# Performance work log

Measured on AMD Instinct MI355X. Metric: run time of the kernel, lower is better.

The kernel has to match this reference:

```python
import jax, jax.numpy as jnp
import numpy as np
from jax.scipy.special import logsumexp

B, S, D, L = 64, 512, 1024, 9


def setup_inputs() -> dict:
    key = jax.random.key(0)
    k1, k2, k3, k4, k5, k6 = jax.random.split(key, 6)
    inputs = jax.random.normal(k1, (B, S, D), dtype=jnp.float32)
    targets = jax.random.randint(k2, (B, S), 0, L)
    sequence_lengths = jax.random.randint(k3, (B,), S // 2, S + 1)
    mask = (jnp.arange(S)[None, :] < sequence_lengths[:, None])
    W = jax.random.normal(k4, (D, L), dtype=jnp.float32) * (1.0 / np.sqrt(D))
    b = jnp.zeros((L,), dtype=jnp.float32)
    transitions = jax.random.normal(k5, (L, L), dtype=jnp.float32) * 0.1
    return {"inputs": inputs, "targets": targets, "sequence_lengths": sequence_lengths,
            "mask": mask, "W": W, "b": b, "transitions": transitions}


def crf_nll(logits, tags, mask, transitions):
    # logits: [B,S,L], tags: [B,S] int, mask: [B,S] bool, transitions: [L,L]
    maskf = mask.astype(logits.dtype)
    # gold-path score (numerator)
    emit = jnp.take_along_axis(logits, tags[..., None], axis=2)[..., 0]  # [B,S]
    trans = transitions[tags[:, :-1], tags[:, 1:]]                        # [B,S-1]
    numerator = (emit * maskf).sum(-1) + (trans * maskf[:, 1:]).sum(-1)   # [B]
    # partition function via forward algorithm (scan over time)
    alpha0 = logits[:, 0]  # [B,L]; position 0 always valid
    emit_t = jnp.swapaxes(logits[:, 1:], 0, 1)   # [S-1,B,L]
    mask_t = jnp.swapaxes(mask[:, 1:], 0, 1)     # [S-1,B]

    def step(alpha, xs):
        e, m = xs
        scores = alpha[:, :, None] + transitions[None, :, :] + e[:, None, :]  # [B,L,L]
        new = logsumexp(scores, axis=1)                                        # [B,L]
        alpha = jnp.where(m[:, None], new, alpha)
        return alpha, None

    alpha, _ = jax.lax.scan(step, alpha0, (emit_t, mask_t))
    denominator = logsumexp(alpha, axis=-1)  # [B]
    return -(numerator - denominator).sum()


def reference(inputs, targets, sequence_lengths, mask, W, b, transitions):
    logits = jnp.einsum('bsd,dl->bsl', inputs, W) + b  # nn.Linear
    values = crf_nll(logits, targets, mask, transitions)
    return (values, logits)
```

## Files before the change

kernel.cpp:

```cpp
#include <hip/hip_runtime.h>
#include <hip/hip_bf16.h>
#include <math.h>

#define BB 64
#define SS 512
#define DD 1024
#define LL 9
#define NCHUNK 32
#define CLEN 16

#define DPP_ADD(v, ctrl)                                                     \
  v += __int_as_float(__builtin_amdgcn_update_dpp(                           \
      0, __float_as_int(v), ctrl, 0xF, 0xF, false))

__global__ __launch_bounds__(256) void gemm_kernel(
    const float* __restrict__ in, const float* __restrict__ W,
    const float* __restrict__ bias, float* __restrict__ out) {
  __shared__ float Wt[LL][DD];
  int tid = threadIdx.x;
  for (int i = tid; i < DD * LL; i += 256) {
    int k = i / LL, l = i - k * LL;
    Wt[l][k] = W[i];
  }
  __syncthreads();

  int lane = tid & 63;
  int wave = tid >> 6;
  int p = lane & 15;
  int sub = lane >> 4;

  int r0 = blockIdx.x * 64 + wave * 16 + sub;
  const float* x0 = in + (size_t)r0 * DD + p * 4;

  float acc[4][LL];
#pragma unroll
  for (int q = 0; q < 4; ++q)
#pragma unroll
    for (int l = 0; l < LL; ++l) acc[q][l] = 0.f;

  float4 a[4], an[4];
#pragma unroll
  for (int q = 0; q < 4; ++q)
    a[q] = *reinterpret_cast<const float4*>(x0 + (size_t)q * 4 * DD);

  for (int it = 0; it < 16; ++it) {
    if (it < 15) {
#pragma unroll
      for (int q = 0; q < 4; ++q)
        an[q] = *reinterpret_cast<const float4*>(x0 + (size_t)q * 4 * DD +
                                                 (it + 1) * 64);
    }
    int k0 = it * 64 + p * 4;
    float4 w4[LL];
#pragma unroll
    for (int l = 0; l < LL; ++l)
      w4[l] = *reinterpret_cast<const float4*>(&Wt[l][k0]);
#pragma unroll
    for (int q = 0; q < 4; ++q)
#pragma unroll
      for (int l = 0; l < LL; ++l)
        acc[q][l] += a[q].x * w4[l].x + a[q].y * w4[l].y + a[q].z * w4[l].z +
                     a[q].w * w4[l].w;
    if (it < 15) {
#pragma unroll
      for (int q = 0; q < 4; ++q) a[q] = an[q];
    }
  }

#pragma unroll
  for (int q = 0; q < 4; ++q)
#pragma unroll
    for (int l = 0; l < LL; ++l) {
      DPP_ADD(acc[q][l], 0x111);
      DPP_ADD(acc[q][l], 0x112);
      DPP_ADD(acc[q][l], 0x114);
      DPP_ADD(acc[q][l], 0x118);
    }
  if (p == 15) {
#pragma unroll
    for (int q = 0; q < 4; ++q)
#pragma unroll
      for (int l = 0; l < LL; ++l)
        out[(size_t)(r0 + q * 4) * LL + l] = acc[q][l] + bias[l];
  }
}

template <int R>
__device__ inline float swz(float x) {
  return __int_as_float(
      __builtin_amdgcn_ds_swizzle(__float_as_int(x), (R << 10) | 0x1F));
}

__global__ __launch_bounds__(64) void crf_chunk_kernel(
    const float* __restrict__ logits, const int* __restrict__ targets,
    const int* __restrict__ seqlen, const float* __restrict__ trans,
    float* __restrict__ mats, float* __restrict__ scales,
    float* __restrict__ numpart, unsigned* __restrict__ counter) {
  if (blockIdx.x == 0 && threadIdx.x == 0) *counter = 0u;

  int lane = threadIdx.x;
  int j = lane & 15;
  int gid = blockIdx.x * 4 + (lane >> 4);
  int b = gid >> 5;
  int k = gid & 31;
  int len = seqlen[b];

  float Mx[81];
#pragma unroll
  for (int i = 0; i < 81; ++i) Mx[i] = __expf(trans[i]);

  float T[LL];
#pragma unroll
  for (int c = 0; c < LL; ++c) T[c] = (j == c) ? 1.f : 0.f;
  float Cl = 0.f;

  const float* lb = logits + (size_t)b * SS * LL;
  const int* tb = targets + (size_t)b * SS;
  int t0 = k * CLEN + 1;
  int tend = (t0 + CLEN < SS) ? (t0 + CLEN) : SS;

  float e[LL];
#pragma unroll
  for (int c = 0; c < LL; ++c) e[c] = lb[t0 * LL + c];

  for (int t = t0; t < tend; ++t) {
    float Ex[LL];
#pragma unroll
    for (int c = 0; c < LL; ++c) Ex[c] = __expf(e[c]);
    if (t + 1 < tend) {
#pragma unroll
      for (int c = 0; c < LL; ++c) e[c] = lb[(t + 1) * LL + c];
    }
    bool active = (t < len);
    float nT[LL];
#pragma unroll
    for (int c = 0; c < LL; ++c) {
      float s = 0.f;
#pragma unroll
      for (int m = 0; m < LL; ++m) s += T[m] * Mx[m * LL + c];
      nT[c] = s * Ex[c];
    }
#pragma unroll
    for (int c = 0; c < LL; ++c) T[c] = active ? nT[c] : T[c];

    if (((t - t0) & 7) == 7) {
      float m = T[0];
#pragma unroll
      for (int c = 1; c < LL; ++c) m = fmaxf(m, T[c]);
      m = fmaxf(m, swz<1>(m));
      m = fmaxf(m, swz<2>(m));
      m = fmaxf(m, swz<4>(m));
      m = fmaxf(m, swz<8>(m));
      float inv = 1.f / m;
#pragma unroll
      for (int c = 0; c < LL; ++c) T[c] *= inv;
      Cl += __logf(m);
    }
  }
  {
    float m = T[0];
#pragma unroll
    for (int c = 1; c < LL; ++c) m = fmaxf(m, T[c]);
    m = fmaxf(m, swz<1>(m));
    m = fmaxf(m, swz<2>(m));
    m = fmaxf(m, swz<4>(m));
    m = fmaxf(m, swz<8>(m));
    float inv = 1.f / m;
#pragma unroll
    for (int c = 0; c < LL; ++c) T[c] *= inv;
    Cl += __logf(m);
  }

  float* Mg = mats + (size_t)gid * 256;
#pragma unroll
  for (int c = 0; c < 16; ++c)
    Mg[c * 16 + (j ^ c)] = (c < LL) ? T[c] : 0.f;
  if (j == 0) scales[gid] = Cl;

  int t = t0 + j;
  float np = 0.f;
  if (t < tend && t < len) {
    int tg = tb[t];
    np = lb[t * LL + tg] + trans[tb[t - 1] * LL + tg];
  }
  np += swz<1>(np);
  np += swz<2>(np);
  np += swz<4>(np);
  np += swz<8>(np);
  if (j == 0) numpart[gid] = np;
}

__global__ __launch_bounds__(64) void crf_combine_kernel(
    const float* __restrict__ logits, const int* __restrict__ targets,
    const float* __restrict__ mats, const float* __restrict__ scales,
    const float* __restrict__ numpart, float* __restrict__ partials,
    unsigned* __restrict__ counter, float* __restrict__ out_val) {
  int lane = threadIdx.x;
  int j = lane & 15;
  int b = blockIdx.x;
  const float* lb = logits + (size_t)b * SS * LL;
  const float* Mb = mats + (size_t)b * NCHUNK * 256;

  float extra = (lane < NCHUNK) ? scales[b * NCHUNK + lane]
                                : -numpart[b * NCHUNK + (lane - 32)];
  extra += __shfl_xor(extra, 1, 64);
  extra += __shfl_xor(extra, 2, 64);
  extra += __shfl_xor(extra, 4, 64);
  extra += __shfl_xor(extra, 8, 64);
  extra += __shfl_xor(extra, 16, 64);
  extra += __shfl_xor(extra, 32, 64);
  float emit0 = lb[targets[(size_t)b * SS]];

  float alpha = (j < LL) ? __expf(lb[j]) : 0.f;
  float C = 0.f;

  float4 c0 = *reinterpret_cast<const float4*>(Mb + j * 16 + 0);
  float4 c1 = *reinterpret_cast<const float4*>(Mb + j * 16 + 4);
  float4 c2 = *reinterpret_cast<const float4*>(Mb + j * 16 + 8);
  float4 c3 = *reinterpret_cast<const float4*>(Mb + j * 16 + 12);

  for (int k = 0; k < NCHUNK; ++k) {
    float4 n0, n1, n2, n3;
    if (k + 1 < NCHUNK) {
      const float* Mn = Mb + (size_t)(k + 1) * 256 + j * 16;
      n0 = *reinterpret_cast<const float4*>(Mn + 0);
      n1 = *reinterpret_cast<const float4*>(Mn + 4);
      n2 = *reinterpret_cast<const float4*>(Mn + 8);
      n3 = *reinterpret_cast<const float4*>(Mn + 12);
    }
    float s01 = alpha * c0.x + swz<1>(alpha) * c0.y;
    float s23 = swz<2>(alpha) * c0.z + swz<3>(alpha) * c0.w;
    float s45 = swz<4>(alpha) * c1.x + swz<5>(alpha) * c1.y;
    float s67 = swz<6>(alpha) * c1.z + swz<7>(alpha) * c1.w;
    float s89 = swz<8>(alpha) * c2.x + swz<9>(alpha) * c2.y;
    float sab = swz<10>(alpha) * c2.z + swz<11>(alpha) * c2.w;
    float scd = swz<12>(alpha) * c3.x + swz<13>(alpha) * c3.y;
    float sef = swz<14>(alpha) * c3.z + swz<15>(alpha) * c3.w;
    alpha = ((s01 + s23) + (s45 + s67)) + ((s89 + sab) + (scd + sef));

    if ((k & 3) == 3) {
      float m = alpha;
      m = fmaxf(m, swz<1>(m));
      m = fmaxf(m, swz<2>(m));
      m = fmaxf(m, swz<4>(m));
      m = fmaxf(m, swz<8>(m));
      float inv = 1.f / m;
      alpha *= inv;
      C += __logf(m);
    }
    if (k + 1 < NCHUNK) { c0 = n0; c1 = n1; c2 = n2; c3 = n3; }
  }

  float s = alpha;
  s += swz<1>(s);
  s += swz<2>(s);
  s += swz<4>(s);
  s += swz<8>(s);
  float result = extra + C + __logf(s) - emit0;

  if (lane == 0) partials[b] = result;
  __threadfence();
  unsigned old = 0;
  if (lane == 0) old = atomicAdd(counter, 1u);
  old = __shfl(old, 0, 64);
  if (old == BB - 1) {
    __threadfence();
    float v = partials[lane];
    v += __shfl_xor(v, 1, 64);
    v += __shfl_xor(v, 2, 64);
    v += __shfl_xor(v, 4, 64);
    v += __shfl_xor(v, 8, 64);
    v += __shfl_xor(v, 16, 64);
    v += __shfl_xor(v, 32, 64);
    if (lane == 0) {
      out_val[0] = v;
      *counter = 0u;
    }
  }
}

extern "C" void kernel_launch(void* const* d_in, const int* in_sizes, int n_in,
                              void* d_out, int out_size, void* d_ws,
                              size_t ws_size, hipStream_t stream) {
  const float* inputs = (const float*)d_in[0];
  const int* targets = (const int*)d_in[1];
  const int* seqlen = (const int*)d_in[2];
  const float* W = (const float*)d_in[4];
  const float* bias = (const float*)d_in[5];
  const float* trans = (const float*)d_in[6];
  float* out = (float*)d_out;

  float* mats = (float*)d_ws;
  float* scales = mats + (size_t)BB * NCHUNK * 256;
  float* numpart = scales + (size_t)BB * NCHUNK;
  float* partials = numpart + (size_t)BB * NCHUNK;
  unsigned* counter = (unsigned*)(partials + BB);

  gemm_kernel<<<512, 256, 0, stream>>>(inputs, W, bias, out + 1);
  crf_chunk_kernel<<<BB * NCHUNK / 4, 64, 0, stream>>>(
      out + 1, targets, seqlen, trans, mats, scales, numpart, counter);
  crf_combine_kernel<<<BB, 64, 0, stream>>>(out + 1, targets, mats, scales,
                                            numpart, partials, counter, out);
}
```

Before: 53.52 us.

## Fuse CRF chunk transfer-matrix computation into GEMM kernel via shared-memory logits

Merges the logits GEMM and the per-chunk CRF transfer-matrix kernel into one launch. Each GEMM block covers 64 timesteps of one sequence, keeps its logits in shared memory, and then uses wave 0 to build four 16-step chunk matrices and wave 1 to compute the gold-path numerator partial for the block. This removes one kernel launch and the global-memory round trip of logits between stages. The cost is a serialized tail in which only one or two waves per block do the chunk scan while the others sit idle.

```diff
diff --git a/kernel.cpp b/kernel.cpp
--- a/kernel.cpp
+++ b/kernel.cpp
@@ -7,17 +7,30 @@
 #define DD 1024
 #define LL 9
 #define NCHUNK 32
-#define CLEN 16
 
 #define DPP_ADD(v, ctrl)                                                     \
   v += __int_as_float(__builtin_amdgcn_update_dpp(                           \
       0, __float_as_int(v), ctrl, 0xF, 0xF, false))
 
-__global__ __launch_bounds__(256) void gemm_kernel(
+template <int R>
+__device__ inline float swz(float x) {
+  return __int_as_float(
+      __builtin_amdgcn_ds_swizzle(__float_as_int(x), (R << 10) | 0x1F));
+}
+
+__global__ __launch_bounds__(256) void fused_kernel(
     const float* __restrict__ in, const float* __restrict__ W,
-    const float* __restrict__ bias, float* __restrict__ out) {
+    const float* __restrict__ bias, const int* __restrict__ targets,
+    const int* __restrict__ seqlen, const float* __restrict__ trans,
+    float* __restrict__ logits, float* __restrict__ mats,
+    float* __restrict__ scales, float* __restrict__ numblk,
+    unsigned* __restrict__ counter) {
   __shared__ float Wt[LL][DD];
+  __shared__ float Lg[64][LL];
   int tid = threadIdx.x;
+  int bid = blockIdx.x;
+  if (bid == 0 && tid == 0) *counter = 0u;
+
   for (int i = tid; i < DD * LL; i += 256) {
     int k = i / LL, l = i - k * LL;
     Wt[l][k] = W[i];
@@ -29,7 +42,7 @@
   int p = lane & 15;
   int sub = lane >> 4;
 
-  int r0 = blockIdx.x * 64 + wave * 16 + sub;
+  int r0 = bid * 64 + wave * 16 + sub;
   const float* x0 = in + (size_t)r0 * DD + p * 4;
 
   float acc[4][LL];
@@ -80,70 +93,75 @@
 #pragma unroll
     for (int q = 0; q < 4; ++q)
 #pragma unroll
-      for (int l = 0; l < LL; ++l)
-        out[(size_t)(r0 + q * 4) * LL + l] = acc[q][l] + bias[l];
-  }
-}
-
-template <int R>
-__device__ inline float swz(float x) {
-  return __int_as_float(
-      __builtin_amdgcn_ds_swizzle(__float_as_int(x), (R << 10) | 0x1F));
-}
-
-__global__ __launch_bounds__(64) void crf_chunk_kernel(
-    const float* __restrict__ logits, const int* __restrict__ targets,
-    const int* __restrict__ seqlen, const float* __restrict__ trans,
-    float* __restrict__ mats, float* __restrict__ scales,
-    float* __restrict__ numpart, unsigned* __restrict__ counter) {
-  if (blockIdx.x == 0 && threadIdx.x == 0) *counter = 0u;
-
-  int lane = threadIdx.x;
-  int j = lane & 15;
-  int gid = blockIdx.x * 4 + (lane >> 4);
-  int b = gid >> 5;
-  int k = gid & 31;
+      for (int l = 0; l < LL; ++l) {
+        float v = acc[q][l] + bias[l];
+        logits[(size_t)(r0 + q * 4) * LL + l] = v;
+        Lg[wave * 16 + sub + q * 4][l] = v;
+      }
+  }
+  __syncthreads();
+
+  int b = bid >> 3;
+  int base = (bid & 7) * 64;
   int len = seqlen[b];
 
-  float Mx[81];
-#pragma unroll
-  for (int i = 0; i < 81; ++i) Mx[i] = __expf(trans[i]);
-
-  float T[LL];
-#pragma unroll
-  for (int c = 0; c < LL; ++c) T[c] = (j == c) ? 1.f : 0.f;
-  float Cl = 0.f;
-
-  const float* lb = logits + (size_t)b * SS * LL;
-  const int* tb = targets + (size_t)b * SS;
-  int t0 = k * CLEN + 1;
-  int tend = (t0 + CLEN < SS) ? (t0 + CLEN) : SS;
-
-  float e[LL];
-#pragma unroll
-  for (int c = 0; c < LL; ++c) e[c] = lb[t0 * LL + c];
-
-  for (int t = t0; t < tend; ++t) {
-    float Ex[LL];
-#pragma unroll
-    for (int c = 0; c < LL; ++c) Ex[c] = __expf(e[c]);
-    if (t + 1 < tend) {
-#pragma unroll
-      for (int c = 0; c < LL; ++c) e[c] = lb[(t + 1) * LL + c];
-    }
-    bool active = (t < len);
-    float nT[LL];
-#pragma unroll
-    for (int c = 0; c < LL; ++c) {
-      float s = 0.f;
-#pragma unroll
-      for (int m = 0; m < LL; ++m) s += T[m] * Mx[m * LL + c];
-      nT[c] = s * Ex[c];
-    }
-#pragma unroll
-    for (int c = 0; c < LL; ++c) T[c] = active ? nT[c] : T[c];
-
-    if (((t - t0) & 7) == 7) {
+  if (wave == 0) {
+    int j = lane & 15;
+    int g = lane >> 4;
+    int kk = (bid & 7) * 4 + g;
+    int gid = b * NCHUNK + kk;
+
+    float Mx[81];
+#pragma unroll
+    for (int i = 0; i < 81; ++i) Mx[i] = __expf(trans[i]);
+
+    float T[LL];
+#pragma unroll
+    for (int c = 0; c < LL; ++c) T[c] = (j == c) ? 1.f : 0.f;
+    float Cl = 0.f;
+
+    int tstart = (kk == 0) ? 1 : kk * 16;
+    int tend = kk * 16 + 16;
+
+    float e[LL];
+#pragma unroll
+    for (int c = 0; c < LL; ++c) e[c] = Lg[tstart - base][c];
+
+    for (int t = tstart; t < tend; ++t) {
+      float Ex[LL];
+#pragma unroll
+      for (int c = 0; c < LL; ++c) Ex[c] = __expf(e[c]);
+      if (t + 1 < tend) {
+#pragma unroll
+        for (int c = 0; c < LL; ++c) e[c] = Lg[t + 1 - base][c];
+      }
+      bool active = (t < len);
+      float nT[LL];
+#pragma unroll
+      for (int c = 0; c < LL; ++c) {
+        float s = 0.f;
+#pragma unroll
+        for (int m = 0; m < LL; ++m) s += T[m] * Mx[m * LL + c];
+        nT[c] = s * Ex[c];
+      }
+#pragma unroll
+      for (int c = 0; c < LL; ++c) T[c] = active ? nT[c] : T[c];
+
+      if (((t - tstart) & 7) == 7) {
+        float m = T[0];
+#pragma unroll
+        for (int c = 1; c < LL; ++c) m = fmaxf(m, T[c]);
+        m = fmaxf(m, swz<1>(m));
+        m = fmaxf(m, swz<2>(m));
+        m = fmaxf(m, swz<4>(m));
+        m = fmaxf(m, swz<8>(m));
+        float inv = 1.f / m;
+#pragma unroll
+        for (int c = 0; c < LL; ++c) T[c] *= inv;
+        Cl += __logf(m);
+      }
+    }
+    {
       float m = T[0];
 #pragma unroll
       for (int c = 1; c < LL; ++c) m = fmaxf(m, T[c]);
@@ -156,44 +174,34 @@
       for (int c = 0; c < LL; ++c) T[c] *= inv;
       Cl += __logf(m);
     }
-  }
-  {
-    float m = T[0];
-#pragma unroll
-    for (int c = 1; c < LL; ++c) m = fmaxf(m, T[c]);
-    m = fmaxf(m, swz<1>(m));
-    m = fmaxf(m, swz<2>(m));
-    m = fmaxf(m, swz<4>(m));
-    m = fmaxf(m, swz<8>(m));
-    float inv = 1.f / m;
-#pragma unroll
-    for (int c = 0; c < LL; ++c) T[c] *= inv;
-    Cl += __logf(m);
-  }
-
-  float* Mg = mats + (size_t)gid * 256;
-#pragma unroll
-  for (int c = 0; c < 16; ++c)
-    Mg[c * 16 + (j ^ c)] = (c < LL) ? T[c] : 0.f;
-  if (j == 0) scales[gid] = Cl;
-
-  int t = t0 + j;
-  float np = 0.f;
-  if (t < tend && t < len) {
-    int tg = tb[t];
-    np = lb[t * LL + tg] + trans[tb[t - 1] * LL + tg];
-  }
-  np += swz<1>(np);
-  np += swz<2>(np);
-  np += swz<4>(np);
-  np += swz<8>(np);
-  if (j == 0) numpart[gid] = np;
+
+    float* Mg = mats + (size_t)gid * 256;
+#pragma unroll
+    for (int c = 0; c < 16; ++c)
+      Mg[c * 16 + (j ^ c)] = (c < LL) ? T[c] : 0.f;
+    if (j == 0) scales[gid] = Cl;
+  } else if (wave == 1) {
+    int t = base + lane;
+    float np = 0.f;
+    const int* tb = targets + (size_t)b * SS;
+    if (t >= 1 && t < len) {
+      int tg = tb[t];
+      np = Lg[lane][tg] + trans[tb[t - 1] * LL + tg];
+    }
+    np += __shfl_xor(np, 1, 64);
+    np += __shfl_xor(np, 2, 64);
+    np += __shfl_xor(np, 4, 64);
+    np += __shfl_xor(np, 8, 64);
+    np += __shfl_xor(np, 16, 64);
+    np += __shfl_xor(np, 32, 64);
+    if (lane == 0) numblk[bid] = np;
+  }
 }
 
 __global__ __launch_bounds__(64) void crf_combine_kernel(
     const float* __restrict__ logits, const int* __restrict__ targets,
     const float* __restrict__ mats, const float* __restrict__ scales,
-    const float* __restrict__ numpart, float* __restrict__ partials,
+    const float* __restrict__ numblk, float* __restrict__ partials,
     unsigned* __restrict__ counter, float* __restrict__ out_val) {
   int lane = threadIdx.x;
   int j = lane & 15;
@@ -201,8 +209,9 @@
   const float* lb = logits + (size_t)b * SS * LL;
   const float* Mb = mats + (size_t)b * NCHUNK * 256;
 
-  float extra = (lane < NCHUNK) ? scales[b * NCHUNK + lane]
-                                : -numpart[b * NCHUNK + (lane - 32)];
+  float extra = 0.f;
+  if (lane < NCHUNK) extra = scales[b * NCHUNK + lane];
+  else if (lane < NCHUNK + 8) extra = -numblk[b * 8 + (lane - NCHUNK)];
   extra += __shfl_xor(extra, 1, 64);
   extra += __shfl_xor(extra, 2, 64);
   extra += __shfl_xor(extra, 4, 64);
@@ -292,13 +301,13 @@
 
   float* mats = (float*)d_ws;
   float* scales = mats + (size_t)BB * NCHUNK * 256;
-  float* numpart = scales + (size_t)BB * NCHUNK;
-  float* partials = numpart + (size_t)BB * NCHUNK;
+  float* numblk = scales + (size_t)BB * NCHUNK;
+  float* partials = numblk + 512;
   unsigned* counter = (unsigned*)(partials + BB);
 
-  gemm_kernel<<<512, 256, 0, stream>>>(inputs, W, bias, out + 1);
-  crf_chunk_kernel<<<BB * NCHUNK / 4, 64, 0, stream>>>(
-      out + 1, targets, seqlen, trans, mats, scales, numpart, counter);
+  fused_kernel<<<512, 256, 0, stream>>>(inputs, W, bias, targets, seqlen,
+                                        trans, out + 1, mats, scales, numblk,
+                                        counter);
   crf_combine_kernel<<<BB, 64, 0, stream>>>(out + 1, targets, mats, scales,
-                                            numpart, partials, counter, out);
+                                            numblk, partials, counter, out);
 }
```

After: 52.96 us. No clear change (-1.0%).

## Hold W in registers and reduce each GEMM row across the full wave

Applied to the files above, without the earlier changes.

The projection GEMM no longer stages W into shared memory. Each lane keeps its 16×9 slice of W in registers (36 float4 values) and processes one row at a time, covering 16 consecutive input columns. The per-row partial sums are then reduced across all 64 lanes with DPP, including row_bcast steps, and lane 63 writes the logits. This removes the LDS staging and the block-level sync, but adds many more cross-lane reduction ops per row and much higher register pressure, which could lower occupancy for a memory-bound kernel.

```diff
diff --git a/kernel.cpp b/kernel.cpp
--- a/kernel.cpp
+++ b/kernel.cpp
@@ -12,83 +12,85 @@
 #define DPP_ADD(v, ctrl)                                                     \
   v += __int_as_float(__builtin_amdgcn_update_dpp(                           \
       0, __float_as_int(v), ctrl, 0xF, 0xF, false))
-
-__global__ __launch_bounds__(256) void gemm_kernel(
-    const float* __restrict__ in, const float* __restrict__ W,
-    const float* __restrict__ bias, float* __restrict__ out) {
-  __shared__ float Wt[LL][DD];
-  int tid = threadIdx.x;
-  for (int i = tid; i < DD * LL; i += 256) {
-    int k = i / LL, l = i - k * LL;
-    Wt[l][k] = W[i];
-  }
-  __syncthreads();
-
-  int lane = tid & 63;
-  int wave = tid >> 6;
-  int p = lane & 15;
-  int sub = lane >> 4;
-
-  int r0 = blockIdx.x * 64 + wave * 16 + sub;
-  const float* x0 = in + (size_t)r0 * DD + p * 4;
-
-  float acc[4][LL];
-#pragma unroll
-  for (int q = 0; q < 4; ++q)
-#pragma unroll
-    for (int l = 0; l < LL; ++l) acc[q][l] = 0.f;
-
-  float4 a[4], an[4];
-#pragma unroll
-  for (int q = 0; q < 4; ++q)
-    a[q] = *reinterpret_cast<const float4*>(x0 + (size_t)q * 4 * DD);
-
-  for (int it = 0; it < 16; ++it) {
-    if (it < 15) {
-#pragma unroll
-      for (int q = 0; q < 4; ++q)
-        an[q] = *reinterpret_cast<const float4*>(x0 + (size_t)q * 4 * DD +
-                                                 (it + 1) * 64);
-    }
-    int k0 = it * 64 + p * 4;
-    float4 w4[LL];
-#pragma unroll
-    for (int l = 0; l < LL; ++l)
-      w4[l] = *reinterpret_cast<const float4*>(&Wt[l][k0]);
-#pragma unroll
-    for (int q = 0; q < 4; ++q)
-#pragma unroll
-      for (int l = 0; l < LL; ++l)
-        acc[q][l] += a[q].x * w4[l].x + a[q].y * w4[l].y + a[q].z * w4[l].z +
-                     a[q].w * w4[l].w;
-    if (it < 15) {
-#pragma unroll
-      for (int q = 0; q < 4; ++q) a[q] = an[q];
-    }
-  }
-
-#pragma unroll
-  for (int q = 0; q < 4; ++q)
-#pragma unroll
-    for (int l = 0; l < LL; ++l) {
-      DPP_ADD(acc[q][l], 0x111);
-      DPP_ADD(acc[q][l], 0x112);
-      DPP_ADD(acc[q][l], 0x114);
-      DPP_ADD(acc[q][l], 0x118);
-    }
-  if (p == 15) {
-#pragma unroll
-    for (int q = 0; q < 4; ++q)
-#pragma unroll
-      for (int l = 0; l < LL; ++l)
-        out[(size_t)(r0 + q * 4) * LL + l] = acc[q][l] + bias[l];
-  }
-}
+#define WAVE_RED63(v)                                                        \
+  do {                                                                       \
+    DPP_ADD(v, 0x111);                                                       \
+    DPP_ADD(v, 0x112);                                                       \
+    DPP_ADD(v, 0x114);                                                       \
+    DPP_ADD(v, 0x118);                                                       \
+    DPP_ADD(v, 0x142);                                                       \
+    DPP_ADD(v, 0x143);                                                       \
+  } while (0)
+
+#define GETC(v, c)                                                           \
+  ((c) == 0 ? (v).x : (c) == 1 ? (v).y : (c) == 2 ? (v).z : (v).w)
 
 template <int R>
 __device__ inline float swz(float x) {
   return __int_as_float(
       __builtin_amdgcn_ds_swizzle(__float_as_int(x), (R << 10) | 0x1F));
+}
+
+__global__ __launch_bounds__(256, 2) void gemm_kernel(
+    const float* __restrict__ in, const float* __restrict__ W,
+    const float* __restrict__ bias, float* __restrict__ out) {
+  int tid = threadIdx.x;
+  int lane = tid & 63;
+  int wave = tid >> 6;
+
+  float4 wf[36];
+  {
+    const float* wsrc = W + (size_t)lane * (16 * LL);
+#pragma unroll
+    for (int j = 0; j < 36; ++j)
+      wf[j] = *reinterpret_cast<const float4*>(wsrc + j * 4);
+  }
+  float bv[LL];
+#pragma unroll
+  for (int l = 0; l < LL; ++l) bv[l] = bias[l];
+
+  int rbase = blockIdx.x * 64 + wave * 16;
+  const float* src = in + (size_t)rbase * DD + lane * 16;
+
+  float4 a[4], an[4];
+#pragma unroll
+  for (int c = 0; c < 4; ++c)
+    a[c] = *reinterpret_cast<const float4*>(src + c * 4);
+
+  for (int ri = 0; ri < 16; ++ri) {
+    if (ri < 15) {
+      const float* nsrc = src + (size_t)(ri + 1) * DD;
+#pragma unroll
+      for (int c = 0; c < 4; ++c)
+        an[c] = *reinterpret_cast<const float4*>(nsrc + c * 4);
+    }
+
+    float acc[LL];
+#pragma unroll
+    for (int l = 0; l < LL; ++l) acc[l] = 0.f;
+#pragma unroll
+    for (int i = 0; i < 16; ++i) {
+      float av = GETC(a[i >> 2], i & 3);
+#pragma unroll
+      for (int l = 0; l < LL; ++l) {
+        const int idx = i * LL + l;
+        acc[l] += av * GETC(wf[idx >> 2], idx & 3);
+      }
+    }
+
+#pragma unroll
+    for (int l = 0; l < LL; ++l) WAVE_RED63(acc[l]);
+    if (lane == 63) {
+      float* g = out + (size_t)(rbase + ri) * LL;
+#pragma unroll
+      for (int l = 0; l < LL; ++l) g[l] = acc[l] + bv[l];
+    }
+
+    if (ri < 15) {
+#pragma unroll
+      for (int c = 0; c < 4; ++c) a[c] = an[c];
+    }
+  }
 }
 
 __global__ __launch_bounds__(64) void crf_chunk_kernel(
```

Result: slower. 59.04 us (+10.3%).
